# Performance work log

Measured on AMD Instinct MI355X. Metric: run time of the kernel, lower is better.

## Reference

```python
import jax, jax.numpy as jnp
import numpy as np

ZETA = 1.1
GAMMA = -0.1

B, F, D = 1024, 32, 128


def setup_inputs() -> dict:
    key = jax.random.key(0)
    k1, k2 = jax.random.split(key)
    feature = jax.random.normal(k1, (B, F, D), dtype=jnp.float32)
    # nn.Parameter init: normal(mean=0, std=0.001)
    matrix = jax.random.normal(k2, (F, F, D, D), dtype=jnp.float32) * 0.001
    return {"feature": feature, "matrix": matrix}


def reference(feature, matrix):
    # feature: [B, F, D]; matrix (logAlpha of hard-concrete gate): [F, F, D, D]
    nF = matrix.shape[0]
    # strict upper-triangular pair mask over (i, j)
    mask = jnp.triu(jnp.ones((nF, nF), dtype=feature.dtype), k=1)
    # deterministic (eval-mode) hard-concrete gate: stretch + clamp
    s = jax.nn.sigmoid(matrix)
    z = jnp.clip(s * (ZETA - GAMMA) + GAMMA, 0.0, 1.0)
    l0_out = mask[:, :, None, None] * z  # [F, F, D, D]
    # out[b,i,j] = f_i^T Z_ij f_j  == sum_{d,e} f[b,i,d] * Z[i,j,d,e] * f[b,j,e]
    # (faithful to: (f[:, :, None, :, None] @ f[:, None, :, None, :]) * Z, summed over (d, e))
    out = jnp.einsum('bid,ijde,bje->bij', feature, l0_out, feature)
    return out
```

## Files before the change

### kernel.cpp

```cpp
#include <hip/hip_runtime.h>

#define F_SZ 32
#define D_SZ 128
#define FD   4096
#define NPAIR 496

typedef __bf16 bf16x8 __attribute__((ext_vector_type(8)));
typedef float floatx4 __attribute__((ext_vector_type(4)));

__device__ __forceinline__ unsigned short f2bf(float f) {
  unsigned u = __float_as_uint(f);
  u += 0x7fffu + ((u >> 16) & 1u);
  return (unsigned short)(u >> 16);
}

__device__ __forceinline__ void decode_pair(int p, int& io, int& jo) {
  int i = 0;
  while (p >= F_SZ - 1 - i) { p -= F_SZ - 1 - i; ++i; }
  io = i; jo = i + 1 + p;
}

__global__ __launch_bounds__(256)
void prep_z(const float* __restrict__ mat, unsigned short* __restrict__ Zt) {
  __shared__ unsigned short tile[128 * 136];
  int i, j; decode_pair(blockIdx.x, i, j);
  const float* zp = mat + (((size_t)i * F_SZ + j) << 14);
  const int t = threadIdx.x;
  #pragma unroll 8
  for (int it = 0; it < 64; ++it) {
    int idx = it * 256 + t;
    int d = idx >> 7, e = idx & 127;
    float v = zp[idx];
    float s = 1.0f / (1.0f + __expf(-v));
    float z = fminf(1.0f, fmaxf(0.0f, fmaf(s, 1.2f, -0.1f)));
    tile[e * 136 + d] = f2bf(z);
  }
  __syncthreads();
  unsigned short* op = Zt + ((size_t)blockIdx.x << 14);
  #pragma unroll 4
  for (int it = 0; it < 16; ++it) {
    int idx4 = it * 256 + t;
    int e = idx4 >> 5, d4 = idx4 & 31;
    ushort4 v = *(const ushort4*)&tile[e * 136 + d4 * 4];
    *(ushort4*)&op[idx4 * 4] = v;
  }
}

__global__ __launch_bounds__(256)
void prep_f(const float* __restrict__ feat, unsigned short* __restrict__ fb) {
  int gid = blockIdx.x * 256 + threadIdx.x;
  #pragma unroll
  for (int k = 0; k < 4; ++k) {
    size_t idx = (size_t)k * 262144 + gid;
    float4 v = *(const float4*)(feat + idx * 4);
    ushort4 h;
    h.x = f2bf(v.x); h.y = f2bf(v.y); h.z = f2bf(v.z); h.w = f2bf(v.w);
    *(ushort4*)(fb + idx * 4) = h;
  }
}

__global__ __launch_bounds__(256, 2)
void pair_gemm(const unsigned short* __restrict__ Zt,
               const unsigned short* __restrict__ fb,
               const float* __restrict__ feat,
               float* __restrict__ out) {
  __shared__ float sRed[128];
  int i, j; decode_pair(blockIdx.x, i, j);
  const int t = threadIdx.x;
  const int lane = t & 63, l15 = lane & 15, quad = lane >> 4;
  const int wq = t >> 6, we = wq & 1, wb = wq >> 1;

  bf16x8 Bfrag[4][4];
  {
    const unsigned short* zp = Zt + ((size_t)blockIdx.x << 14);
    #pragma unroll
    for (int nf = 0; nf < 4; ++nf) {
      const int col = we * 64 + nf * 16 + l15;
      #pragma unroll
      for (int ks = 0; ks < 4; ++ks)
        Bfrag[nf][ks] = *(const bf16x8*)(zp + col * 128 + ks * 32 + quad * 8);
    }
  }

  const int bbase = blockIdx.y * 256;
  for (int it = 0; it < 2; ++it) {
    const int b0 = bbase + it * 128;
    const int rowbase = b0 + wb * 64;

    floatx4 acc[4][4];
    #pragma unroll
    for (int mf = 0; mf < 4; ++mf)
      #pragma unroll
      for (int nf = 0; nf < 4; ++nf)
        acc[mf][nf] = (floatx4){0.f, 0.f, 0.f, 0.f};

    #pragma unroll
    for (int ks = 0; ks < 4; ++ks) {
      #pragma unroll
      for (int mf = 0; mf < 4; ++mf) {
        const unsigned short* ap = fb + (size_t)(rowbase + mf * 16 + l15) * FD
                                      + i * D_SZ + ks * 32 + quad * 8;
        bf16x8 A = *(const bf16x8*)ap;
        #pragma unroll
        for (int nf = 0; nf < 4; ++nf)
          acc[mf][nf] = __builtin_amdgcn_mfma_f32_16x16x32_bf16(A, Bfrag[nf][ks], acc[mf][nf], 0, 0, 0);
      }
    }

    float pl[4][4];
    #pragma unroll
    for (int mf = 0; mf < 4; ++mf) {
      #pragma unroll
      for (int r = 0; r < 4; ++r) pl[mf][r] = 0.f;
      #pragma unroll
      for (int nf = 0; nf < 4; ++nf) {
        const int col = we * 64 + nf * 16 + l15;
        const float* fj = feat + (size_t)(rowbase + mf * 16 + quad * 4) * FD + j * D_SZ + col;
        floatx4 c = acc[mf][nf];
        pl[mf][0] += c[0] * fj[0];
        pl[mf][1] += c[1] * fj[FD];
        pl[mf][2] += c[2] * fj[2 * FD];
        pl[mf][3] += c[3] * fj[3 * FD];
      }
    }
    #pragma unroll
    for (int mf = 0; mf < 4; ++mf)
      #pragma unroll
      for (int r = 0; r < 4; ++r)
        #pragma unroll
        for (int off = 1; off < 16; off <<= 1)
          pl[mf][r] += __shfl_xor(pl[mf][r], off, 64);

    if (we == 0 && l15 == 0) {
      #pragma unroll
      for (int mf = 0; mf < 4; ++mf)
        #pragma unroll
        for (int r = 0; r < 4; ++r)
          sRed[wb * 64 + mf * 16 + quad * 4 + r] = pl[mf][r];
    }
    __syncthreads();
    if (we == 1 && l15 == 0) {
      #pragma unroll
      for (int mf = 0; mf < 4; ++mf)
        #pragma unroll
        for (int r = 0; r < 4; ++r) {
          const int lr = wb * 64 + mf * 16 + quad * 4 + r;
          out[(size_t)(b0 + lr) * (F_SZ * F_SZ) + i * F_SZ + j] = pl[mf][r] + sRed[lr];
        }
    }
    __syncthreads();
  }
}

#define LDA  136
#define LDB  136
__device__ __forceinline__ float bf2f(unsigned short h) {
  return __uint_as_float(((unsigned)h) << 16);
}

__global__ __launch_bounds__(256, 2)
void interaction_pair_kernel(const float* __restrict__ feat,
                             const float* __restrict__ mat,
                             float* __restrict__ out) {
  __shared__ unsigned short sA[128 * LDA];
  __shared__ unsigned short sBT[128 * LDB];
  const int t = threadIdx.x;
  const int w = t >> 6, lane = t & 63, l15 = lane & 15, quad = lane >> 4;
  int i, j; decode_pair(blockIdx.x, i, j);
  {
    const float* zp = mat + (((size_t)i * F_SZ + j) << 14);
    #pragma unroll 8
    for (int it = 0; it < 64; ++it) {
      int idx = it * 256 + t;
      int d = idx >> 7, e = idx & 127;
      float v = zp[idx];
      float s = 1.0f / (1.0f + __expf(-v));
      float z = fminf(1.0f, fmaxf(0.0f, fmaf(s, 1.2f, -0.1f)));
      sBT[e * LDB + d] = f2bf(z);
    }
  }
  for (int bt = 0; bt < 8; ++bt) {
    const int b0 = bt * 128;
    #pragma unroll 4
    for (int it = 0; it < 16; ++it) {
      int idx4 = it * 256 + t;
      int r = idx4 >> 5, c4 = idx4 & 31;
      const float4 v = *(const float4*)(feat + (size_t)(b0 + r) * FD + i * D_SZ + c4 * 4);
      ushort4 h;
      h.x = f2bf(v.x); h.y = f2bf(v.y); h.z = f2bf(v.z); h.w = f2bf(v.w);
      *(ushort4*)(&sA[r * LDA + c4 * 4]) = h;
    }
    __syncthreads();
    floatx4 acc[2][8];
    #pragma unroll
    for (int mf = 0; mf < 2; ++mf)
      #pragma unroll
      for (int nf = 0; nf < 8; ++nf)
        acc[mf][nf] = (floatx4){0.f, 0.f, 0.f, 0.f};
    #pragma unroll
    for (int k0 = 0; k0 < 128; k0 += 32) {
      const int kc = k0 + quad * 8;
      bf16x8 a0 = *(const bf16x8*)&sA[(w * 32 +      l15) * LDA + kc];
      bf16x8 a1 = *(const bf16x8*)&sA[(w * 32 + 16 + l15) * LDA + kc];
      #pragma unroll
      for (int nf = 0; nf < 8; ++nf) {
        bf16x8 bfr = *(const bf16x8*)&sBT[(nf * 16 + l15) * LDB + kc];
        acc[0][nf] = __builtin_amdgcn_mfma_f32_16x16x32_bf16(a0, bfr, acc[0][nf], 0, 0, 0);
        acc[1][nf] = __builtin_amdgcn_mfma_f32_16x16x32_bf16(a1, bfr, acc[1][nf], 0, 0, 0);
      }
    }
    #pragma unroll
    for (int mf = 0; mf < 2; ++mf) {
      float pl[4] = {0.f, 0.f, 0.f, 0.f};
      const int rb = w * 32 + mf * 16 + quad * 4;
      #pragma unroll
      for (int nf = 0; nf < 8; ++nf) {
        const int col = nf * 16 + l15;
        const float* fj = feat + (size_t)(b0 + rb) * FD + j * D_SZ + col;
        floatx4 c = acc[mf][nf];
        pl[0] += c[0] * fj[0];
        pl[1] += c[1] * fj[FD];
        pl[2] += c[2] * fj[2 * FD];
        pl[3] += c[3] * fj[3 * FD];
      }
      #pragma unroll
      for (int off = 1; off < 16; off <<= 1) {
        pl[0] += __shfl_xor(pl[0], off, 64);
        pl[1] += __shfl_xor(pl[1], off, 64);
        pl[2] += __shfl_xor(pl[2], off, 64);
        pl[3] += __shfl_xor(pl[3], off, 64);
      }
      if (l15 == 0) {
        size_t ob = (size_t)(b0 + rb) * (F_SZ * F_SZ) + (size_t)i * F_SZ + j;
        out[ob]                   = pl[0];
        out[ob + 1 * F_SZ * F_SZ] = pl[1];
        out[ob + 2 * F_SZ * F_SZ] = pl[2];
        out[ob + 3 * F_SZ * F_SZ] = pl[3];
      }
    }
    __syncthreads();
  }
}

extern "C" void kernel_launch(void* const* d_in, const int* in_sizes, int n_in,
                              void* d_out, int out_size, void* d_ws, size_t ws_size,
                              hipStream_t stream) {
  const float* feat = (const float*)d_in[0];
  const float* mat  = (const float*)d_in[1];
  float* out = (float*)d_out;

  hipMemsetAsync(out, 0, (size_t)out_size * sizeof(float), stream);

  const size_t zt_bytes = (size_t)NPAIR * D_SZ * D_SZ * sizeof(unsigned short);
  const size_t fb_bytes = (size_t)1024 * FD * sizeof(unsigned short);

  if (ws_size >= zt_bytes + fb_bytes) {
    unsigned short* Zt = (unsigned short*)d_ws;
    unsigned short* fbuf = Zt + (size_t)NPAIR * D_SZ * D_SZ;
    prep_z<<<dim3(NPAIR), dim3(256), 0, stream>>>(mat, Zt);
    prep_f<<<dim3(1024), dim3(256), 0, stream>>>(feat, fbuf);
    pair_gemm<<<dim3(NPAIR, 4), dim3(256), 0, stream>>>(Zt, fbuf, feat, out);
  } else {
    interaction_pair_kernel<<<dim3(NPAIR), dim3(256), 0, stream>>>(feat, mat, out);
  }
}
```

Baseline: 171.7 us.

## Transpose pair GEMM operands, vectorize epilogue, use atomics and fewer batch blocks

```diff
diff --git a/kernel.cpp b/kernel.cpp
--- a/kernel.cpp
+++ b/kernel.cpp
@@ -64,28 +64,27 @@
                const unsigned short* __restrict__ fb,
                const float* __restrict__ feat,
                float* __restrict__ out) {
-  __shared__ float sRed[128];
   int i, j; decode_pair(blockIdx.x, i, j);
   const int t = threadIdx.x;
   const int lane = t & 63, l15 = lane & 15, quad = lane >> 4;
   const int wq = t >> 6, we = wq & 1, wb = wq >> 1;
 
-  bf16x8 Bfrag[4][4];
+  bf16x8 Afrag[4][4];
   {
     const unsigned short* zp = Zt + ((size_t)blockIdx.x << 14);
     #pragma unroll
-    for (int nf = 0; nf < 4; ++nf) {
-      const int col = we * 64 + nf * 16 + l15;
+    for (int mf = 0; mf < 4; ++mf) {
+      const int e = we * 64 + mf * 16 + l15;
       #pragma unroll
       for (int ks = 0; ks < 4; ++ks)
-        Bfrag[nf][ks] = *(const bf16x8*)(zp + col * 128 + ks * 32 + quad * 8);
-    }
-  }
-
-  const int bbase = blockIdx.y * 256;
-  for (int it = 0; it < 2; ++it) {
-    const int b0 = bbase + it * 128;
-    const int rowbase = b0 + wb * 64;
+        Afrag[mf][ks] = *(const bf16x8*)(zp + e * 128 + ks * 32 + quad * 8);
+    }
+  }
+
+  const int bbase = blockIdx.y * 512;
+  #pragma unroll 1
+  for (int it = 0; it < 4; ++it) {
+    const int rowbase = bbase + it * 128 + wb * 64;
 
     floatx4 acc[4][4];
     #pragma unroll
@@ -96,67 +95,44 @@
 
     #pragma unroll
     for (int ks = 0; ks < 4; ++ks) {
-      #pragma unroll
-      for (int mf = 0; mf < 4; ++mf) {
-        const unsigned short* ap = fb + (size_t)(rowbase + mf * 16 + l15) * FD
-                                      + i * D_SZ + ks * 32 + quad * 8;
-        bf16x8 A = *(const bf16x8*)ap;
+      bf16x8 Bf[4];
+      #pragma unroll
+      for (int nf = 0; nf < 4; ++nf)
+        Bf[nf] = *(const bf16x8*)(fb + (size_t)(rowbase + nf * 16 + l15) * FD
+                                     + i * D_SZ + ks * 32 + quad * 8);
+      #pragma unroll
+      for (int mf = 0; mf < 4; ++mf)
         #pragma unroll
         for (int nf = 0; nf < 4; ++nf)
-          acc[mf][nf] = __builtin_amdgcn_mfma_f32_16x16x32_bf16(A, Bfrag[nf][ks], acc[mf][nf], 0, 0, 0);
-      }
-    }
-
-    float pl[4][4];
-    #pragma unroll
-    for (int mf = 0; mf < 4; ++mf) {
-      #pragma unroll
-      for (int r = 0; r < 4; ++r) pl[mf][r] = 0.f;
-      #pragma unroll
-      for (int nf = 0; nf < 4; ++nf) {
-        const int col = we * 64 + nf * 16 + l15;
-        const float* fj = feat + (size_t)(rowbase + mf * 16 + quad * 4) * FD + j * D_SZ + col;
-        floatx4 c = acc[mf][nf];
-        pl[mf][0] += c[0] * fj[0];
-        pl[mf][1] += c[1] * fj[FD];
-        pl[mf][2] += c[2] * fj[2 * FD];
-        pl[mf][3] += c[3] * fj[3 * FD];
-      }
-    }
-    #pragma unroll
-    for (int mf = 0; mf < 4; ++mf)
-      #pragma unroll
-      for (int r = 0; r < 4; ++r)
-        #pragma unroll
-        for (int off = 1; off < 16; off <<= 1)
-          pl[mf][r] += __shfl_xor(pl[mf][r], off, 64);
-
-    if (we == 0 && l15 == 0) {
-      #pragma unroll
-      for (int mf = 0; mf < 4; ++mf)
-        #pragma unroll
-        for (int r = 0; r < 4; ++r)
-          sRed[wb * 64 + mf * 16 + quad * 4 + r] = pl[mf][r];
-    }
-    __syncthreads();
-    if (we == 1 && l15 == 0) {
-      #pragma unroll
-      for (int mf = 0; mf < 4; ++mf)
-        #pragma unroll
-        for (int r = 0; r < 4; ++r) {
-          const int lr = wb * 64 + mf * 16 + quad * 4 + r;
-          out[(size_t)(b0 + lr) * (F_SZ * F_SZ) + i * F_SZ + j] = pl[mf][r] + sRed[lr];
-        }
-    }
-    __syncthreads();
+          acc[mf][nf] = __builtin_amdgcn_mfma_f32_16x16x32_bf16(Afrag[mf][ks], Bf[nf], acc[mf][nf], 0, 0, 0);
+    }
+
+    #pragma unroll
+    for (int nf = 0; nf < 4; ++nf) {
+      const int b = rowbase + nf * 16 + l15;
+      const float* fjp = feat + (size_t)b * FD + j * D_SZ + we * 64 + quad * 4;
+      float4 fj0 = *(const float4*)(fjp);
+      float4 fj1 = *(const float4*)(fjp + 16);
+      float4 fj2 = *(const float4*)(fjp + 32);
+      float4 fj3 = *(const float4*)(fjp + 48);
+      float pl;
+      {
+        floatx4 c0 = acc[0][nf], c1 = acc[1][nf], c2 = acc[2][nf], c3 = acc[3][nf];
+        pl  = c0[0] * fj0.x + c0[1] * fj0.y + c0[2] * fj0.z + c0[3] * fj0.w;
+        pl += c1[0] * fj1.x + c1[1] * fj1.y + c1[2] * fj1.z + c1[3] * fj1.w;
+        pl += c2[0] * fj2.x + c2[1] * fj2.y + c2[2] * fj2.z + c2[3] * fj2.w;
+        pl += c3[0] * fj3.x + c3[1] * fj3.y + c3[2] * fj3.z + c3[3] * fj3.w;
+      }
+      pl += __shfl_xor(pl, 16, 64);
+      pl += __shfl_xor(pl, 32, 64);
+      if (quad == 0)
+        atomicAdd(&out[(size_t)b * (F_SZ * F_SZ) + i * F_SZ + j], pl);
+    }
   }
 }
 
 #define LDA  136
 #define LDB  136
-__device__ __forceinline__ float bf2f(unsigned short h) {
-  return __uint_as_float(((unsigned)h) << 16);
-}
 
 __global__ __launch_bounds__(256, 2)
 void interaction_pair_kernel(const float* __restrict__ feat,
@@ -259,7 +235,7 @@
     unsigned short* fbuf = Zt + (size_t)NPAIR * D_SZ * D_SZ;
     prep_z<<<dim3(NPAIR), dim3(256), 0, stream>>>(mat, Zt);
     prep_f<<<dim3(1024), dim3(256), 0, stream>>>(feat, fbuf);
-    pair_gemm<<<dim3(NPAIR, 4), dim3(256), 0, stream>>>(Zt, fbuf, feat, out);
+    pair_gemm<<<dim3(NPAIR, 2), dim3(256), 0, stream>>>(Zt, fbuf, feat, out);
   } else {
     interaction_pair_kernel<<<dim3(NPAIR), dim3(256), 0, stream>>>(feat, mat, out);
   }
```

Measured after the change: 188.5 us. +9.8%, slower.
